# Optimization experiments

Hardware: AMD Instinct MI355X
Metric: run time of the kernel (lower is better)

Reference implementation:

```python
import jax, jax.numpy as jnp
import numpy as np
from math import sqrt

# ---- config (mirrors init_kwargs / input_specs) ----
B, N = 2, 2048
DIM, HEADS = 1024, 16
DH = DIM // HEADS
NUM_STEPS = 8
BETA = 1.0
SCALE = sqrt(DIM / 2 - 1)        # scale_from_dim(dim)
SCALE_HEAD = sqrt(DH / 2 - 1)    # scale_from_dim(dim_head)


def _normalize(x, eps=1e-12):
    # torch F.normalize(dim=-1): x / max(||x||, eps)
    n = jnp.linalg.norm(x, axis=-1, keepdims=True)
    return x / jnp.maximum(n, eps)


def _theta(x, J, m):
    # effective field: external field + attention-weighted coupling of magnetizations
    return x + jnp.einsum('bhij,bhjd->bhid', J, m)


def _magnetizations(theta, beta=BETA, scale=SCALE):
    # naive-MF single-site average for a vector spin on a sphere of radius `scale`
    # (steepest-descent closed form): m = beta*theta / (2 t),
    # t = (1 + sqrt(1 + beta^2 |theta|^2 / scale^2)) / 2
    # -> linear response beta*theta/2 for small fields, saturates at |m| = scale.
    h2 = jnp.sum(jnp.square(beta * theta), axis=-1, keepdims=True)
    t = 0.5 * (1.0 + jnp.sqrt(1.0 + h2 / (scale * scale)))
    return beta * theta / (2.0 * t)


def setup_inputs() -> dict:
    key = jax.random.key(0)
    k0, k1, k2, k3 = jax.random.split(key, 4)
    x = jax.random.normal(k0, (B, N, DIM), jnp.float32)
    w_qk = jax.random.normal(k1, (2 * DIM, DIM), jnp.float32) / sqrt(DIM)
    w1 = jax.random.normal(k2, (4 * DIM, DIM), jnp.float32) / sqrt(DIM)
    w2 = jax.random.normal(k3, (DIM, 4 * DIM), jnp.float32) / sqrt(4 * DIM)
    return {"x": x, "w_qk": w_qk, "w1": w1, "w2": w2}


def reference(x, w_qk, w1, w2):
    # pre_mix = Identity
    x = SCALE * _normalize(x)                         # [b,n,dim]
    qk = x @ w_qk.T                                   # [b,n,2*dim]
    q, k = jnp.split(qk, 2, axis=-1)
    ff = jax.nn.gelu(x @ w1.T, approximate=False) @ w2.T

    split = lambda t: t.reshape(B, N, HEADS, DH).transpose(0, 2, 1, 3)  # b h n d
    xh, q, k, ffh = map(split, (x, q, k, ff))
    q, k = _normalize(q), _normalize(k)
    sim = SCALE_HEAD * jnp.einsum('bhid,bhjd->bhij', q, k)
    attn = jax.nn.softmax(sim, axis=-1)               # [b,h,n,n] coupling matrix

    xf = xh + ffh                                     # external field
    # prev_mf_state.theta starts as ones(x.shape) on first call
    m0 = _magnetizations(jnp.ones_like(xf))

    # fixed-step mean-field iteration: m <- magnetizations(theta(x, attn, m))
    def body(m, _):
        m_next = _magnetizations(_theta(xf, attn, m))
        return m_next, None
    m, _ = jax.lax.scan(body, m0, None, length=NUM_STEPS)

    m = m.transpose(0, 2, 1, 3).reshape(B, N, DIM)    # merge heads
    # post_mix = Identity
    return m
```

## Files before the change

### kernel.cpp

```cpp
#include <hip/hip_runtime.h>
#include <hip/hip_bf16.h>
#include <math.h>

#define BQ 2
#define SEQ 2048
#define NDIM 1024
#define HEADS 16
#define DH 64
#define NSTEPS 8
#define SCALE 22.60530911f
#define SCALE_HEAD 5.567764363f
#define INV_SCALE2 (1.0f/511.0f)
#define EXS 8.0325527f

typedef unsigned short u16;
typedef unsigned char u8;
typedef long long i64;
typedef __attribute__((ext_vector_type(8))) short bf16x8;
typedef __attribute__((ext_vector_type(4))) float floatx4;
typedef __attribute__((ext_vector_type(2))) long long i64x2;

__device__ __forceinline__ float bf2f(u16 u) {
  union { unsigned int i; float f; } v; v.i = ((unsigned int)u) << 16; return v.f;
}
__device__ __forceinline__ u16 f2bf(float f) {
  union { float f; unsigned int i; } v; v.f = f;
  unsigned int x = v.i;
  return (u16)((x + 0x7fffu + ((x >> 16) & 1u)) >> 16);
}
#if __has_builtin(__builtin_amdgcn_exp2f)
__device__ __forceinline__ float exp2_raw(float x) { return __builtin_amdgcn_exp2f(x); }
#else
__device__ __forceinline__ float exp2_raw(float x) { return exp2f(x); }
#endif
#if __has_builtin(__builtin_amdgcn_rcpf)
__device__ __forceinline__ float rcp_raw(float x) { return __builtin_amdgcn_rcpf(x); }
#else
__device__ __forceinline__ float rcp_raw(float x) { return 1.0f/x; }
#endif

__device__ __forceinline__ float gelu_tanh(float v) {
  float v2 = v*v;
  float u = v * __builtin_fmaf(0.0356774081f, v2, 0.7978845608f);
  float t = exp2_raw(2.8853900817779268f * u);
  float th = (t - 1.0f) * rcp_raw(t + 1.0f);
  return 0.5f * v * (1.0f + th);
}

__device__ __forceinline__ int pk4_fp8(float a, float b, float c, float d) {
  int p = 0;
  p = __builtin_amdgcn_cvt_pk_fp8_f32(a, b, p, false);
  p = __builtin_amdgcn_cvt_pk_fp8_f32(c, d, p, true);
  return p;
}

#define GLD16(gp, lp) __builtin_amdgcn_global_load_lds( \
    (__attribute__((address_space(1))) void*)(gp),      \
    (__attribute__((address_space(3))) void*)(lp), 16, 0, 0)


__global__ void k_flag0(int* flag) { if (threadIdx.x == 0 && blockIdx.x == 0) *flag = 0; }

__global__ __launch_bounds__(256) void k_probe(const u16* __restrict__ x, int* __restrict__ flag) {
  int i = blockIdx.x * 256 + threadIdx.x;
  float v = bf2f(x[i]);
  if (!(fabsf(v) <= 1e4f)) atomicOr(flag, 1);
}

__global__ __launch_bounds__(256) void k_convert(const void* __restrict__ in, u16* __restrict__ outb,
                                                 const int* __restrict__ flag, int n) {
  int i = blockIdx.x * 256 + threadIdx.x;
  if (i >= n) return;
  if (*flag) outb[i] = f2bf(((const float*)in)[i]);
  else       outb[i] = ((const u16*)in)[i];
}

__global__ __launch_bounds__(256) void k_norm_scale(const u16* __restrict__ x, u16* __restrict__ xs) {
  __shared__ float red[256];
  int row = blockIdx.x;
  const u16* xr = x + (size_t)row * NDIM;
  u16* orow = xs + (size_t)row * NDIM;
  int t = threadIdx.x;
  float vals[4]; float s = 0.f;
#pragma unroll
  for (int e = 0; e < 4; e++) { float v = bf2f(xr[t + 256*e]); vals[e] = v; s += v*v; }
  red[t] = s; __syncthreads();
  for (int o = 128; o > 0; o >>= 1) { if (t < o) red[t] += red[t+o]; __syncthreads(); }
  float sc = SCALE / fmaxf(sqrtf(red[0]), 1e-12f);
#pragma unroll
  for (int e = 0; e < 4; e++) orow[t + 256*e] = f2bf(vals[e] * sc);
}

template<int OUT_BF16, int GELU, int ADDSRC>
__global__ __launch_bounds__(256) void k_gemm(const u16* __restrict__ A, const u16* __restrict__ W,
                                              float* __restrict__ Cf, u16* __restrict__ Cb,
                                              const u16* __restrict__ addsrc, int M, int N, int K) {
  __shared__ __align__(16) u16 As[2][128*32];
  __shared__ __align__(16) u16 Bs[2][128*32];
  int t = threadIdx.x;
  int w = t >> 6, L = t & 63;
  int quad = L >> 4, l15 = L & 15;
  int wr = w >> 1, wc = w & 1;
  int bm = blockIdx.x * 128, bn = blockIdx.y * 128;
  int srow = L >> 2, scol = (L & 3) * 8;
  floatx4 acc[4][4];
#pragma unroll
  for (int i = 0; i < 4; i++)
#pragma unroll
    for (int j = 0; j < 4; j++) acc[i][j] = (floatx4){0.f,0.f,0.f,0.f};

  for (int k0 = 0; k0 < K; k0 += 64) {
#pragma unroll
    for (int c = 0; c < 2; c++) {
      int r = c*64 + w*16 + srow;
      const u16* ap = A + (size_t)(bm + r)*K + k0 + scol;
      const u16* wp = W + (size_t)(bn + r)*K + k0 + scol;
      GLD16(ap,      &As[0][(c*64 + w*16)*32]);
      GLD16(ap + 32, &As[1][(c*64 + w*16)*32]);
      GLD16(wp,      &Bs[0][(c*64 + w*16)*32]);
      GLD16(wp + 32, &Bs[1][(c*64 + w*16)*32]);
    }
    __syncthreads();
#pragma unroll
    for (int s = 0; s < 2; s++) {
      bf16x8 af[4], bfr[4];
#pragma unroll
      for (int mt = 0; mt < 4; mt++) af[mt]  = *(const bf16x8*)&As[s][(wr*64 + mt*16 + l15)*32 + quad*8];
#pragma unroll
      for (int nt = 0; nt < 4; nt++) bfr[nt] = *(const bf16x8*)&Bs[s][(wc*64 + nt*16 + l15)*32 + quad*8];
#pragma unroll
      for (int mt = 0; mt < 4; mt++)
#pragma unroll
        for (int nt = 0; nt < 4; nt++)
          acc[mt][nt] = __builtin_amdgcn_mfma_f32_16x16x32_bf16(af[mt], bfr[nt], acc[mt][nt], 0, 0, 0);
    }
    __syncthreads();
  }
#pragma unroll
  for (int mt = 0; mt < 4; mt++)
#pragma unroll
    for (int reg = 0; reg < 4; reg++) {
      int m = bm + wr*64 + mt*16 + quad*4 + reg;
      size_t rowoff = (size_t)m * N;
#pragma unroll
      for (int nt = 0; nt < 4; nt++) {
        int n = bn + wc*64 + nt*16 + l15;
        float v = acc[mt][nt][reg];
        if (GELU) v = gelu_tanh(v);
        if (ADDSRC) v += bf2f(addsrc[rowoff + n]);
        if (OUT_BF16) Cb[rowoff + n] = f2bf(v);
        else Cf[rowoff + n] = v;
      }
    }
}

__global__ __launch_bounds__(512) void k_gemm_w2(const u16* __restrict__ A, const u16* __restrict__ W,
                                                 float* __restrict__ Cf,
                                                 const u16* __restrict__ addsrc, int M, int N, int K) {
  __shared__ __align__(16) u16 As[2][128*32];
  __shared__ __align__(16) u16 Bs[2][128*32];
  int t = threadIdx.x;
  int g = t >> 8;
  int tg = t & 255;
  int w = tg >> 6;
  int L = t & 63;
  int quad = L >> 4, l15 = L & 15;
  int wr = w >> 1, wc = w & 1;
  int bm = blockIdx.x * 128, bn = blockIdx.y * 128;
  int srow = L >> 2, scol = (L & 3) * 8;
  int kg0 = g * (K >> 1);
  floatx4 acc[4][4];
#pragma unroll
  for (int i = 0; i < 4; i++)
#pragma unroll
    for (int j = 0; j < 4; j++) acc[i][j] = (floatx4){0.f,0.f,0.f,0.f};

  for (int k0 = 0; k0 < (K >> 1); k0 += 32) {
    int kk = kg0 + k0;
#pragma unroll
    for (int c = 0; c < 2; c++) {
      int r = c*64 + w*16 + srow;
      GLD16(A + (size_t)(bm + r)*K + kk + scol, &As[g][(c*64 + w*16)*32]);
      GLD16(W + (size_t)(bn + r)*K + kk + scol, &Bs[g][(c*64 + w*16)*32]);
    }
    __syncthreads();
    bf16x8 af[4], bfr[4];
#pragma unroll
    for (int mt = 0; mt < 4; mt++) af[mt]  = *(const bf16x8*)&As[g][(wr*64 + mt*16 + l15)*32 + quad*8];
#pragma unroll
    for (int nt = 0; nt < 4; nt++) bfr[nt] = *(const bf16x8*)&Bs[g][(wc*64 + nt*16 + l15)*32 + quad*8];
#pragma unroll
    for (int mt = 0; mt < 4; mt++)
#pragma unroll
      for (int nt = 0; nt < 4; nt++)
        acc[mt][nt] = __builtin_amdgcn_mfma_f32_16x16x32_bf16(af[mt], bfr[nt], acc[mt][nt], 0, 0, 0);
    __syncthreads();
  }
  float* LFA = (float*)&As[0][0];
  float* LFB = (float*)&Bs[0][0];
#pragma unroll
  for (int r = 0; r < 2; r++) {
    float* myW = g ? LFA : LFB;
    int mtW = g ? r : (2 + r);
#pragma unroll
    for (int reg = 0; reg < 4; reg++)
#pragma unroll
      for (int nt = 0; nt < 4; nt++)
        myW[(wr*16 + quad*4 + reg)*128 + wc*64 + nt*16 + l15] = acc[mtW][nt][reg];
    __syncthreads();
    float* myR = g ? LFB : LFA;
    int mtS = g ? (2 + r) : r;
#pragma unroll
    for (int reg = 0; reg < 4; reg++) {
      int m = bm + wr*64 + mtS*16 + quad*4 + reg;
      size_t rowoff = (size_t)m * N;
#pragma unroll
      for (int nt = 0; nt < 4; nt++) {
        int n = bn + wc*64 + nt*16 + l15;
        float v = acc[mtS][nt][reg] + myR[(wr*16 + quad*4 + reg)*128 + wc*64 + nt*16 + l15];
        v += bf2f(addsrc[rowoff + n]);
        Cf[rowoff + n] = v;
      }
    }
    __syncthreads();
  }
}

__global__ __launch_bounds__(512) void k_gemm_w2ks(const u16* __restrict__ A, const u16* __restrict__ W,
                                                   float* __restrict__ pbuf, int M, int N, int K) {
  __shared__ __align__(16) u16 As[2][128*32];
  __shared__ __align__(16) u16 Bs[2][128*32];
  int t = threadIdx.x;
  int g = t >> 8;
  int tg = t & 255;
  int w = tg >> 6;
  int L = t & 63;
  int quad = L >> 4, l15 = L & 15;
  int wr = w >> 1, wc = w & 1;
  int bm = blockIdx.x * 128, bn = blockIdx.y * 128;
  int z = blockIdx.z;
  int srow = L >> 2, scol = (L & 3) * 8;
  int kg0 = z * (K >> 1) + g * (K >> 2);
  floatx4 acc[4][4];
#pragma unroll
  for (int i = 0; i < 4; i++)
#pragma unroll
    for (int j = 0; j < 4; j++) acc[i][j] = (floatx4){0.f,0.f,0.f,0.f};

  for (int k0 = 0; k0 < (K >> 2); k0 += 32) {
    int kk = kg0 + k0;
#pragma unroll
    for (int c = 0; c < 2; c++) {
      int r = c*64 + w*16 + srow;
      GLD16(A + (size_t)(bm + r)*K + kk + scol, &As[g][(c*64 + w*16)*32]);
      GLD16(W + (size_t)(bn + r)*K + kk + scol, &Bs[g][(c*64 + w*16)*32]);
    }
    __syncthreads();
    bf16x8 af[4], bfr[4];
#pragma unroll
    for (int mt = 0; mt < 4; mt++) af[mt]  = *(const bf16x8*)&As[g][(wr*64 + mt*16 + l15)*32 + quad*8];
#pragma unroll
    for (int nt = 0; nt < 4; nt++) bfr[nt] = *(const bf16x8*)&Bs[g][(wc*64 + nt*16 + l15)*32 + quad*8];
#pragma unroll
    for (int mt = 0; mt < 4; mt++)
#pragma unroll
      for (int nt = 0; nt < 4; nt++)
        acc[mt][nt] = __builtin_amdgcn_mfma_f32_16x16x32_bf16(af[mt], bfr[nt], acc[mt][nt], 0, 0, 0);
    __syncthreads();
  }
  float* LFA = (float*)&As[0][0];
  float* LFB = (float*)&Bs[0][0];
  float* pb = pbuf + (size_t)z * M * N;
#pragma unroll
  for (int r = 0; r < 2; r++) {
    float* myW = g ? LFA : LFB;
    int mtW = g ? r : (2 + r);
#pragma unroll
    for (int reg = 0; reg < 4; reg++)
#pragma unroll
      for (int nt = 0; nt < 4; nt++)
        myW[(wr*16 + quad*4 + reg)*128 + wc*64 + nt*16 + l15] = acc[mtW][nt][reg];
    __syncthreads();
    float* myR = g ? LFB : LFA;
    int mtS = g ? (2 + r) : r;
#pragma unroll
    for (int reg = 0; reg < 4; reg++) {
      int m = bm + wr*64 + mtS*16 + quad*4 + reg;
      size_t rowoff = (size_t)m * N;
#pragma unroll
      for (int nt = 0; nt < 4; nt++) {
        int n = bn + wc*64 + nt*16 + l15;
        pb[rowoff + n] = acc[mtS][nt][reg] + myR[(wr*16 + quad*4 + reg)*128 + wc*64 + nt*16 + l15];
      }
    }
    __syncthreads();
  }
}

__global__ __launch_bounds__(256) void k_w2red(const float* __restrict__ p0, const float* __restrict__ p1,
                                               const u16* __restrict__ xs, float* __restrict__ xf, int n) {
  int i = (blockIdx.x * 256 + threadIdx.x) * 4;
  if (i >= n) return;
  float4 a = *(const float4*)(p0 + i);
  float4 b = *(const float4*)(p1 + i);
  ushort4 s = *(const ushort4*)(xs + i);
  float4 o;
  o.x = a.x + b.x + bf2f(s.x);
  o.y = a.y + b.y + bf2f(s.y);
  o.z = a.z + b.z + bf2f(s.z);
  o.w = a.w + b.w + bf2f(s.w);
  *(float4*)(xf + i) = o;
}

__global__ __launch_bounds__(64) void k_headnorm(const u16* __restrict__ qkraw,
                                                 u16* __restrict__ qn, u16* __restrict__ kn) {
  int blk = blockIdx.x;
  int h = blk & (HEADS-1); int bi = blk >> 4;
  int b = bi >> 11, i = bi & (SEQ-1);
  int d = threadIdx.x;
  const u16* base = qkraw + (size_t)bi * (2*NDIM);
  float qv = bf2f(base[h*DH + d]);
  float kv = bf2f(base[NDIM + h*DH + d]);
  float qs = qv*qv, ks = kv*kv;
#pragma unroll
  for (int o = 32; o > 0; o >>= 1) { qs += __shfl_xor(qs, o); ks += __shfl_xor(ks, o); }
  size_t oidx = ((size_t)(b*HEADS + h) * SEQ + i) * DH + d;
  qn[oidx] = f2bf(qv / fmaxf(sqrtf(qs), 1e-12f));
  kn[oidx] = f2bf(kv / fmaxf(sqrtf(ks), 1e-12f));
}

__global__ __launch_bounds__(256, 4) void k_attn(const u16* __restrict__ qb, const u16* __restrict__ kb,
                                                 u8* __restrict__ attn, float* __restrict__ rowsum,
                                                 int bh0, int CH) {
  __shared__ __align__(16) u8 buf[4][4][64][16];
  __shared__ float reds[4][4][16];
  int t = threadIdx.x;
  int w = t >> 6, L = t & 63;
  int quad = L >> 4, l15 = L & 15;
  int blk = blockIdx.x;
  int bh_local, islice;
  if (CH >= 8) {
    int gpb = CH >> 3;
    int q = blk >> 3;
    bh_local = (blk & 7) + 8 * (q % gpb);
    islice = q / gpb;
  } else {
    bh_local = blk >> 5;
    islice = blk & 31;
  }
  int bh = bh0 + bh_local;
  int i0blk = islice * 64;
  bf16x8 q0[4], q1[4];
#pragma unroll
  for (int s = 0; s < 4; s++) {
    const u16* qrow = qb + ((size_t)bh*SEQ + i0blk + s*16 + l15)*DH + quad*8;
    q0[s] = *(const bf16x8*)qrow;
    q1[s] = *(const bf16x8*)(qrow + 32);
  }
  const u16* kbase = kb + (size_t)bh*SEQ*DH;
  u8* abase = attn + ((size_t)bh_local << 22) + (size_t)(i0blk >> 4)*32768;
  float sa[4] = {0.f, 0.f, 0.f, 0.f};
  for (int g = 0; g < 8; g++) {
#pragma unroll 2
    for (int tt4 = 0; tt4 < 4; tt4++) {
      int j = w*512 + (g*4 + tt4)*16 + l15;
      const u16* krow = kbase + (size_t)j*DH + quad*8;
      bf16x8 a0 = *(const bf16x8*)krow;
      bf16x8 a1 = *(const bf16x8*)(krow + 32);
      int dl = ((tt4*2 + (quad>>1)) & 3)*16 + l15;
      int boff = (tt4>>1)*8 + (quad&1)*4;
      floatx4 cs[4];
      __builtin_amdgcn_s_setprio(1);
#pragma unroll
      for (int s = 0; s < 4; s++) {
        floatx4 c = (floatx4){0.f,0.f,0.f,0.f};
        c = __builtin_amdgcn_mfma_f32_16x16x32_bf16(a0, q0[s], c, 0, 0, 0);
        cs[s] = __builtin_amdgcn_mfma_f32_16x16x32_bf16(a1, q1[s], c, 0, 0, 0);
      }
      __builtin_amdgcn_s_setprio(0);
#pragma unroll
      for (int s = 0; s < 4; s++) {
        float e0 = exp2_raw(EXS * cs[s][0]);
        float e1 = exp2_raw(EXS * cs[s][1]);
        float e2 = exp2_raw(EXS * cs[s][2]);
        float e3 = exp2_raw(EXS * cs[s][3]);
        sa[s] += (e0 + e1) + (e2 + e3);
        *(int*)&buf[w][s][dl][boff] = pk4_fp8(e0, e1, e2, e3);
      }
    }
#pragma unroll
    for (int s = 0; s < 4; s++) {
      uint4 v = *(const uint4*)&buf[w][s][L][0];
      *(uint4*)(abase + (size_t)s*32768 + (size_t)(w*8 + g)*1024 + (size_t)L*16) = v;
    }
  }
#pragma unroll
  for (int s = 0; s < 4; s++) {
    float v = sa[s];
    v += __shfl_xor(v, 16); v += __shfl_xor(v, 32);
    if (quad == 0) reds[w][s][l15] = v;
  }
  __syncthreads();
  if (t < 64)
    rowsum[(size_t)bh_local*SEQ + i0blk + t] =
        (reds[0][t >> 4][t & 15] + reds[1][t >> 4][t & 15]) +
        (reds[2][t >> 4][t & 15] + reds[3][t >> 4][t & 15]);
}

__global__ void k_zero(float* __restrict__ o, int n) {
  int i = blockIdx.x*256 + threadIdx.x; if (i < n) o[i] = 0.f;
}

__global__ __launch_bounds__(256) void k_step0(const float* __restrict__ xf, u8* __restrict__ mT,
                                               float m0v) {
  __shared__ __align__(16) u8 tile_t[64][72];
  int bh = blockIdx.x >> 5;
  int kt2 = blockIdx.x & 31;
  int i0 = kt2 * 64;
  int b = bh >> 4, h = bh & (HEADS-1);
  int t = threadIdx.x;
  int row = t >> 2, part = t & 3;
  const float* xr = xf + ((size_t)b*SEQ + i0 + row)*NDIM + h*DH + part*16;
  float v[16]; float s = 0.f;
#pragma unroll
  for (int e = 0; e < 16; e++) { float u = xr[e] + m0v; v[e] = u; s += u*u; }
  s += __shfl_xor(s, 1); s += __shfl_xor(s, 2);
  float t2 = 0.5f*(1.0f + sqrtf(1.0f + s * INV_SCALE2));
  float inv = 1.0f/(2.0f*t2);
#pragma unroll
  for (int e = 0; e < 16; e += 4) {
    int p = pk4_fp8(v[e]*inv, v[e+1]*inv, v[e+2]*inv, v[e+3]*inv);
    tile_t[part*16 + e + 0][row] = (u8)(p & 255);
    tile_t[part*16 + e + 1][row] = (u8)((p >> 8) & 255);
    tile_t[part*16 + e + 2][row] = (u8)((p >> 16) & 255);
    tile_t[part*16 + e + 3][row] = (u8)((p >> 24) & 255);
  }
  __syncthreads();
  int nt = t >> 6, Lw = t & 63;
  i64 lo = *(const i64*)&tile_t[nt*16 + (Lw & 15)][(Lw >> 4)*8];
  i64 hi = *(const i64*)&tile_t[nt*16 + (Lw & 15)][32 + (Lw >> 4)*8];
  u8* dst = mT + ((size_t)bh << 17) + ((size_t)(nt*32 + kt2)*64 + Lw)*16;
  *(i64*)dst = lo;
  *(i64*)(dst + 8) = hi;
}

template<int LAST>
__global__ __launch_bounds__(256) void k_step(const u8* __restrict__ attn, const u8* __restrict__ mT_in,
                                              const float* __restrict__ xf,
                                              const float* __restrict__ rowsum,
                                              u8* __restrict__ mT_out,
                                              float* __restrict__ out, int bh0, int CH) {
  int t = threadIdx.x;
  int w = t >> 6, L = t & 63;
  int quad = L >> 4, l15 = L & 15;
  int blk = blockIdx.x;
  int bh_local, I4;
  if (CH >= 8) {
    int gpb = CH >> 3;
    int q = blk >> 3;
    bh_local = (blk & 7) + 8 * (q % gpb);
    I4 = q / gpb;
  } else {
    bh_local = blk >> 5;
    I4 = blk & 31;
  }
  int bh = bh0 + bh_local;
  int I = I4*4 + w;
  int b = bh >> 4, hh = bh & (HEADS-1);
  const u8* ab = attn + ((size_t)bh_local << 22) + (size_t)I*32768 + (size_t)L*16;
  const u8* bb = mT_in + ((size_t)bh << 17) + (size_t)L*16;
  floatx4 acc[4];
#pragma unroll
  for (int j = 0; j < 4; j++) acc[j] = (floatx4){0.f,0.f,0.f,0.f};

#pragma unroll 4
  for (int kt2 = 0; kt2 < 32; kt2++) {
    i64x2 a  = *(const i64x2*)(ab + (size_t)kt2*1024);
    i64x2 b0 = *(const i64x2*)(bb + (size_t)kt2*1024);
    i64x2 b1 = *(const i64x2*)(bb + (size_t)(32 + kt2)*1024);
    i64x2 b2 = *(const i64x2*)(bb + (size_t)(64 + kt2)*1024);
    i64x2 b3 = *(const i64x2*)(bb + (size_t)(96 + kt2)*1024);
    __builtin_amdgcn_s_setprio(1);
    acc[0] = __builtin_amdgcn_mfma_f32_16x16x32_fp8_fp8(a.x, b0.x, acc[0], 0, 0, 0);
    acc[1] = __builtin_amdgcn_mfma_f32_16x16x32_fp8_fp8(a.x, b1.x, acc[1], 0, 0, 0);
    acc[2] = __builtin_amdgcn_mfma_f32_16x16x32_fp8_fp8(a.x, b2.x, acc[2], 0, 0, 0);
    acc[3] = __builtin_amdgcn_mfma_f32_16x16x32_fp8_fp8(a.x, b3.x, acc[3], 0, 0, 0);
    acc[0] = __builtin_amdgcn_mfma_f32_16x16x32_fp8_fp8(a.y, b0.y, acc[0], 0, 0, 0);
    acc[1] = __builtin_amdgcn_mfma_f32_16x16x32_fp8_fp8(a.y, b1.y, acc[1], 0, 0, 0);
    acc[2] = __builtin_amdgcn_mfma_f32_16x16x32_fp8_fp8(a.y, b2.y, acc[2], 0, 0, 0);
    acc[3] = __builtin_amdgcn_mfma_f32_16x16x32_fp8_fp8(a.y, b3.y, acc[3], 0, 0, 0);
    __builtin_amdgcn_s_setprio(0);
  }
  int ibase = I*16 + quad*4;
  float th[4][4]; float invr[4];
#pragma unroll
  for (int reg = 0; reg < 4; reg++) {
    float sinv = 1.0f / rowsum[(size_t)bh_local*SEQ + ibase + reg];
    size_t xoff = ((size_t)b*SEQ + ibase + reg)*NDIM + hh*DH + l15;
    float s = 0.f;
#pragma unroll
    for (int nt = 0; nt < 4; nt++) {
      float v = acc[nt][reg]*sinv + xf[xoff + nt*16];
      th[nt][reg] = v; s += v*v;
    }
    s += __shfl_xor(s, 1); s += __shfl_xor(s, 2); s += __shfl_xor(s, 4); s += __shfl_xor(s, 8);
    float tt2 = 0.5f*(1.0f + sqrtf(1.0f + s * INV_SCALE2));
    invr[reg] = 1.0f/(2.0f*tt2);
  }
  if (LAST) {
#pragma unroll
    for (int reg = 0; reg < 4; reg++) {
      size_t ooff = ((size_t)b*SEQ + ibase + reg)*NDIM + hh*DH + l15;
#pragma unroll
      for (int nt = 0; nt < 4; nt++) out[ooff + nt*16] = th[nt][reg]*invr[reg];
    }
  } else {
    int kt2o = I >> 2;
    int hf = (I >> 1) & 1;
    int lhi = ((I & 1)*2 + (quad >> 1)) & 3;
    u8* ob = mT_out + ((size_t)bh << 17) + (size_t)(lhi*16 + l15)*16 + hf*8 + (quad & 1)*4;
#pragma unroll
    for (int nt = 0; nt < 4; nt++) {
      int p = pk4_fp8(th[nt][0]*invr[0], th[nt][1]*invr[1],
                      th[nt][2]*invr[2], th[nt][3]*invr[3]);
      *(int*)(ob + (size_t)(nt*32 + kt2o)*1024) = p;
    }
  }
}

extern "C" void kernel_launch(void* const* d_in, const int* in_sizes, int n_in,
                              void* d_out, int out_size, void* d_ws, size_t ws_size,
                              hipStream_t stream) {
  const void* x    = d_in[0];
  const void* w_qk = d_in[1];
  const void* w1   = d_in[2];
  const void* w2   = d_in[3];
  float* out = (float*)d_out;

  const size_t E = (size_t)BQ*SEQ*NDIM;
  const int NW_QK = 2*NDIM*NDIM;
  const int NW1   = 4*NDIM*NDIM;
  const int NW2   = 4*NDIM*NDIM;

  char* ws = (char*)d_ws;
  size_t off = 0;
  auto alloc = [&](size_t bytes) { void* p = ws + off; off += (bytes + 255) & ~255ull; return p; };
  int*  flag = (int*)alloc(256);
  u16*  xs  = (u16*)alloc(E*2);
  u16*  qb  = (u16*)alloc(E*2);
  u16*  kb  = (u16*)alloc(E*2);
  float* xf = (float*)alloc(E*4);
  u8*   mT  = (u8*)alloc(E*2);
  float* rsum = (float*)alloc((size_t)BQ*HEADS*SEQ*4);
  u8*   mTa = mT;
  u8*   mTb = mT + E;

  char* S = ws + off;
  size_t availS = (ws_size > off) ? ws_size - off : 0;
  u16* wqkb  = (u16*)(S);
  u16* qkraw = (u16*)(S + 4194304);
  u16* w1b   = (u16*)(S + 20971520);
  u16* w2b   = (u16*)(S + 29360128);
  u16* hbuf  = (u16*)(S + 37748736);
  u8*  attn  = (u8*)(S);
  u16* xb    = (u16*)mT;

  const int rcs[6] = {4096, 2048, 1024, 512, 256, 128};
  int RC = 0;
  for (int i = 0; i < 6; i++)
    if (37748736ull + (size_t)rcs[i]*4096*2 <= availS) { RC = rcs[i]; break; }
  const int chs[6] = {32, 16, 8, 4, 2, 1};
  int CH = 0;
  for (int i = 0; i < 6; i++)
    if ((size_t)chs[i]*SEQ*SEQ <= availS) { CH = chs[i]; break; }
  if (RC == 0 || CH == 0) {
    k_zero<<<(out_size+255)/256, 256, 0, stream>>>(out, out_size);
    return;
  }
  size_t pboff = 37748736ull + (size_t)RC*4096*2;
  int use_ksp = (pboff + (size_t)RC*NDIM*8 <= availS) ? 1 : 0;
  float* pbuf = (float*)(S + pboff);

  const int M = BQ*SEQ;

  k_flag0<<<1, 64, 0, stream>>>(flag);
  k_probe<<<256, 256, 0, stream>>>((const u16*)x, flag);
  k_convert<<<(int)(E/256), 256, 0, stream>>>(x, xb, flag, (int)E);
  k_convert<<<NW_QK/256, 256, 0, stream>>>(w_qk, wqkb, flag, NW_QK);
  k_convert<<<NW1/256, 256, 0, stream>>>(w1, w1b, flag, NW1);
  k_convert<<<NW2/256, 256, 0, stream>>>(w2, w2b, flag, NW2);

  k_norm_scale<<<M, 256, 0, stream>>>(xb, xs);
  { dim3 g(M/128, 2048/128); k_gemm<1,0,0><<<g, 256, 0, stream>>>(xs, wqkb, nullptr, qkraw, nullptr, M, 2048, 1024); }
  k_headnorm<<<M*HEADS, 64, 0, stream>>>(qkraw, qb, kb);

  for (int c = 0; c < M/RC; c++) {
    const u16* xsc = xs + (size_t)c*RC*NDIM;
    { dim3 g(RC/128, 4096/128); k_gemm<1,1,0><<<g, 256, 0, stream>>>(xsc, w1b, nullptr, hbuf, nullptr, RC, 4096, 1024); }
    if (use_ksp) {
      dim3 g(RC/128, 1024/128, 2);
      k_gemm_w2ks<<<g, 512, 0, stream>>>(hbuf, w2b, pbuf, RC, 1024, 4096);
      int n = RC*NDIM;
      k_w2red<<<n/1024, 256, 0, stream>>>(pbuf, pbuf + n, xsc, xf + (size_t)c*RC*NDIM, n);
    } else {
      dim3 g(RC/128, 1024/128);
      k_gemm_w2<<<g, 512, 0, stream>>>(hbuf, w2b, xf + (size_t)c*RC*NDIM, xsc, RC, 1024, 4096);
    }
  }

  float t0 = 0.5f*(1.0f + sqrtf(1.0f + 64.0f/511.0f));
  float m0v = 1.0f/(2.0f*t0);
  k_step0<<<BQ*HEADS*32, 256, 0, stream>>>(xf, mTa, m0v);

  for (int c0 = 0; c0 < BQ*HEADS; c0 += CH) {
    k_attn<<<CH*32, 256, 0, stream>>>(qb, kb, attn, rsum, c0, CH);
    for (int s = 1; s < NSTEPS; s++) {
      u8* src = (s & 1) ? mTa : mTb;
      u8* dst = (s & 1) ? mTb : mTa;
      if (s == NSTEPS-1)
        k_step<1><<<CH*32, 256, 0, stream>>>(attn, src, xf, rsum, nullptr, out, c0, CH);
      else
        k_step<0><<<CH*32, 256, 0, stream>>>(attn, src, xf, rsum, dst, nullptr, c0, CH);
    }
  }
}
```

Measured before the change: 515.5 us.

## Fuse input conversion into norm-scale and double K-step in split-K W2 GEMM

The separate x conversion kernel is removed: the norm-scale kernel now reads x directly as fp32 or bf16 depending on the probe flag, saving one pass over the activations and one launch. The split-K W2 GEMM now loads two 32-wide K slabs per iteration into doubled shared buffers, halving the number of barriers per K range at the cost of doubling shared memory (64KB per block), which may reduce occupancy.

```diff
diff --git a/kernel.cpp b/kernel.cpp
--- a/kernel.cpp
+++ b/kernel.cpp
@@ -75,15 +75,23 @@
   else       outb[i] = ((const u16*)in)[i];
 }
 
-__global__ __launch_bounds__(256) void k_norm_scale(const u16* __restrict__ x, u16* __restrict__ xs) {
+__global__ __launch_bounds__(256) void k_norm_scale_f(const void* __restrict__ xin,
+                                                      const int* __restrict__ flag,
+                                                      u16* __restrict__ xs) {
   __shared__ float red[256];
   int row = blockIdx.x;
-  const u16* xr = x + (size_t)row * NDIM;
   u16* orow = xs + (size_t)row * NDIM;
   int t = threadIdx.x;
   float vals[4]; float s = 0.f;
-#pragma unroll
-  for (int e = 0; e < 4; e++) { float v = bf2f(xr[t + 256*e]); vals[e] = v; s += v*v; }
+  if (*flag) {
+    const float* xr = (const float*)xin + (size_t)row * NDIM;
+#pragma unroll
+    for (int e = 0; e < 4; e++) { float v = xr[t + 256*e]; vals[e] = v; s += v*v; }
+  } else {
+    const u16* xr = (const u16*)xin + (size_t)row * NDIM;
+#pragma unroll
+    for (int e = 0; e < 4; e++) { float v = bf2f(xr[t + 256*e]); vals[e] = v; s += v*v; }
+  }
   red[t] = s; __syncthreads();
   for (int o = 128; o > 0; o >>= 1) { if (t < o) red[t] += red[t+o]; __syncthreads(); }
   float sc = SCALE / fmaxf(sqrtf(red[0]), 1e-12f);
@@ -228,8 +236,8 @@
 
 __global__ __launch_bounds__(512) void k_gemm_w2ks(const u16* __restrict__ A, const u16* __restrict__ W,
                                                    float* __restrict__ pbuf, int M, int N, int K) {
-  __shared__ __align__(16) u16 As[2][128*32];
-  __shared__ __align__(16) u16 Bs[2][128*32];
+  __shared__ __align__(16) u16 As[2][2][128*32];
+  __shared__ __align__(16) u16 Bs[2][2][128*32];
   int t = threadIdx.x;
   int g = t >> 8;
   int tg = t & 255;
@@ -247,29 +255,36 @@
 #pragma unroll
     for (int j = 0; j < 4; j++) acc[i][j] = (floatx4){0.f,0.f,0.f,0.f};
 
-  for (int k0 = 0; k0 < (K >> 2); k0 += 32) {
+  for (int k0 = 0; k0 < (K >> 2); k0 += 64) {
     int kk = kg0 + k0;
 #pragma unroll
     for (int c = 0; c < 2; c++) {
       int r = c*64 + w*16 + srow;
-      GLD16(A + (size_t)(bm + r)*K + kk + scol, &As[g][(c*64 + w*16)*32]);
-      GLD16(W + (size_t)(bn + r)*K + kk + scol, &Bs[g][(c*64 + w*16)*32]);
-    }
-    __syncthreads();
-    bf16x8 af[4], bfr[4];
-#pragma unroll
-    for (int mt = 0; mt < 4; mt++) af[mt]  = *(const bf16x8*)&As[g][(wr*64 + mt*16 + l15)*32 + quad*8];
-#pragma unroll
-    for (int nt = 0; nt < 4; nt++) bfr[nt] = *(const bf16x8*)&Bs[g][(wc*64 + nt*16 + l15)*32 + quad*8];
-#pragma unroll
-    for (int mt = 0; mt < 4; mt++)
-#pragma unroll
-      for (int nt = 0; nt < 4; nt++)
-        acc[mt][nt] = __builtin_amdgcn_mfma_f32_16x16x32_bf16(af[mt], bfr[nt], acc[mt][nt], 0, 0, 0);
-    __syncthreads();
-  }
-  float* LFA = (float*)&As[0][0];
-  float* LFB = (float*)&Bs[0][0];
+      const u16* ap = A + (size_t)(bm + r)*K + kk + scol;
+      const u16* wp = W + (size_t)(bn + r)*K + kk + scol;
+      GLD16(ap,      &As[g][0][(c*64 + w*16)*32]);
+      GLD16(ap + 32, &As[g][1][(c*64 + w*16)*32]);
+      GLD16(wp,      &Bs[g][0][(c*64 + w*16)*32]);
+      GLD16(wp + 32, &Bs[g][1][(c*64 + w*16)*32]);
+    }
+    __syncthreads();
+#pragma unroll
+    for (int s = 0; s < 2; s++) {
+      bf16x8 af[4], bfr[4];
+#pragma unroll
+      for (int mt = 0; mt < 4; mt++) af[mt]  = *(const bf16x8*)&As[g][s][(wr*64 + mt*16 + l15)*32 + quad*8];
+#pragma unroll
+      for (int nt = 0; nt < 4; nt++) bfr[nt] = *(const bf16x8*)&Bs[g][s][(wc*64 + nt*16 + l15)*32 + quad*8];
+#pragma unroll
+      for (int mt = 0; mt < 4; mt++)
+#pragma unroll
+        for (int nt = 0; nt < 4; nt++)
+          acc[mt][nt] = __builtin_amdgcn_mfma_f32_16x16x32_bf16(af[mt], bfr[nt], acc[mt][nt], 0, 0, 0);
+    }
+    __syncthreads();
+  }
+  float* LFA = (float*)&As[0][0][0];
+  float* LFB = (float*)&Bs[0][0][0];
   float* pb = pbuf + (size_t)z * M * N;
 #pragma unroll
   for (int r = 0; r < 2; r++) {
@@ -563,7 +578,6 @@
   u16* w2b   = (u16*)(S + 29360128);
   u16* hbuf  = (u16*)(S + 37748736);
   u8*  attn  = (u8*)(S);
-  u16* xb    = (u16*)mT;
 
   const int rcs[6] = {4096, 2048, 1024, 512, 256, 128};
   int RC = 0;
@@ -585,12 +599,11 @@
 
   k_flag0<<<1, 64, 0, stream>>>(flag);
   k_probe<<<256, 256, 0, stream>>>((const u16*)x, flag);
-  k_convert<<<(int)(E/256), 256, 0, stream>>>(x, xb, flag, (int)E);
   k_convert<<<NW_QK/256, 256, 0, stream>>>(w_qk, wqkb, flag, NW_QK);
   k_convert<<<NW1/256, 256, 0, stream>>>(w1, w1b, flag, NW1);
   k_convert<<<NW2/256, 256, 0, stream>>>(w2, w2b, flag, NW2);
 
-  k_norm_scale<<<M, 256, 0, stream>>>(xb, xs);
+  k_norm_scale_f<<<M, 256, 0, stream>>>(x, flag, xs);
   { dim3 g(M/128, 2048/128); k_gemm<1,0,0><<<g, 256, 0, stream>>>(xs, wqkb, nullptr, qkraw, nullptr, M, 2048, 1024); }
   k_headnorm<<<M*HEADS, 64, 0, stream>>>(qkraw, qb, kb);
 
```

Result: faster. 495.3 us (-3.9%).
